# Performance work log

Hardware: AMD Instinct MI355X
Metric: run time of the kernel (lower is better)

Reference implementation:

```python
import jax, jax.numpy as jnp
from jax import lax
import numpy as np

B, T, NX, NXS, NY, NYS, H = 4096, 60, 4, 3, 4, 3, 128


def lstm(x, h0, c0, Wih, Whh, bih, bhh):
    """PyTorch-convention LSTM. x: [B,T,D] -> (hs [B,T,H], hT, cT). Gate order i,f,g,o."""
    xg = jnp.einsum('btd,gd->btg', x, Wih) + bih  # [B,T,4H] precomputed input gates

    def step(carry, xg_t):
        h, c = carry
        g = xg_t + h @ Whh.T + bhh
        i, f, gg, o = jnp.split(g, 4, axis=-1)
        c = jax.nn.sigmoid(f) * c + jax.nn.sigmoid(i) * jnp.tanh(gg)
        h = jax.nn.sigmoid(o) * jnp.tanh(c)
        return (h, c), h

    (hT, cT), hs = lax.scan(step, (h0, c0), jnp.swapaxes(xg, 0, 1))
    return jnp.swapaxes(hs, 0, 1), hT, cT


def setup_inputs() -> dict:
    key = jax.random.key(0)
    ks = jax.random.split(key, 24)
    s = 0.1  # weight init scale
    inp = {
        'inputs_main': jax.random.normal(ks[0], (B, T, NX), jnp.float32),
        'inputs_sfc': jax.random.normal(ks[1], (B, NXS), jnp.float32),
        'rnn1_mem': jax.random.normal(ks[2], (B, T, H), jnp.float32),
        'hx2': jax.random.normal(ks[3], (B, H), jnp.float32),
        'cx2': jax.random.normal(ks[4], (B, H), jnp.float32),
        # surface MLPs -> initial h/c of rnn1
        'W_sfc1': s * jax.random.normal(ks[5], (H, NXS), jnp.float32),
        'b_sfc1': s * jax.random.normal(ks[6], (H,), jnp.float32),
        'W_sfc2': s * jax.random.normal(ks[7], (H, NXS), jnp.float32),
        'b_sfc2': s * jax.random.normal(ks[8], (H,), jnp.float32),
        # rnn1: input dim nx + nh_mem = 4 + 128 = 132
        'Wih1': s * jax.random.normal(ks[9], (4 * H, NX + H), jnp.float32),
        'Whh1': s * jax.random.normal(ks[10], (4 * H, H), jnp.float32),
        'bih1': s * jax.random.normal(ks[11], (4 * H,), jnp.float32),
        'bhh1': s * jax.random.normal(ks[12], (4 * H,), jnp.float32),
        # rnn2: input dim H
        'Wih2': s * jax.random.normal(ks[13], (4 * H, H), jnp.float32),
        'Whh2': s * jax.random.normal(ks[14], (4 * H, H), jnp.float32),
        'bih2': s * jax.random.normal(ks[15], (4 * H,), jnp.float32),
        'bhh2': s * jax.random.normal(ks[16], (4 * H,), jnp.float32),
        # intermediate + output MLPs
        'W_lat': s * jax.random.normal(ks[17], (H, H), jnp.float32),
        'b_lat': s * jax.random.normal(ks[18], (H,), jnp.float32),
        'W_out': s * jax.random.normal(ks[19], (NY, H), jnp.float32),
        'b_out': s * jax.random.normal(ks[20], (NY,), jnp.float32),
        'W_so': s * jax.random.normal(ks[21], (NYS, H), jnp.float32),
        'b_so': s * jax.random.normal(ks[22], (NYS,), jnp.float32),
    }
    return inp


def reference(inputs_main, inputs_sfc, rnn1_mem, hx2, cx2,
              W_sfc1, b_sfc1, W_sfc2, b_sfc2,
              Wih1, Whh1, bih1, bhh1,
              Wih2, Whh2, bih2, bhh2,
              W_lat, b_lat, W_out, b_out, W_so, b_so):
    # initial states of rnn1 from surface features
    hx = jnp.tanh(inputs_sfc @ W_sfc1.T + b_sfc1)
    cx = jnp.tanh(inputs_sfc @ W_sfc2.T + b_sfc2)
    # flip vertical levels, concat memory feedback
    x = jnp.flip(inputs_main, axis=1)
    x = jnp.concatenate([x, rnn1_mem], axis=2)  # [B,T,NX+H]
    rnn1out, _, _ = lstm(x, hx, cx, Wih1, Whh1, bih1, bhh1)
    rnn1out = jnp.flip(rnn1out, axis=1)
    # second LSTM over the opposite direction, random initial state
    rnn2out, last_h, _ = lstm(rnn1out, hx2, cx2, Wih2, Whh2, bih2, bhh2)
    # intermediate mlp (also becomes next-step memory in the stateful module)
    lat = rnn2out @ W_lat.T + b_lat  # [B,T,H]
    out = lat @ W_out.T + b_out      # [B,T,NY]
    out_sfc = last_h @ W_so.T + b_so  # [B,NYS]
    return out, out_sfc
```

## Files before the change

kernel.cpp:

```cpp
#include <hip/hip_runtime.h>
#include <stdint.h>


typedef __bf16 bf16x8 __attribute__((ext_vector_type(8)));
typedef __bf16 bf16x4 __attribute__((ext_vector_type(4)));
typedef float  f32x4  __attribute__((ext_vector_type(4)));

#define HQ      4096u
#define H0_OFF  0u
#define XD_OFF  8192u
#define XA_OFF  16384u
#define HIST    24064u
#define LDS_SZ  163328
#define NWS     26

#define S1f (-1.4426950408889634f)
#define S2f (-2.8853900817779268f)

__device__ __forceinline__ bf16x8 ldw8s(const float* __restrict__ p, float s){
  float4 a = *(const float4*)p;
  float4 b = *(const float4*)(p+4);
  bf16x8 r;
  r[0]=(__bf16)(a.x*s); r[1]=(__bf16)(a.y*s); r[2]=(__bf16)(a.z*s); r[3]=(__bf16)(a.w*s);
  r[4]=(__bf16)(b.x*s); r[5]=(__bf16)(b.y*s); r[6]=(__bf16)(b.z*s); r[7]=(__bf16)(b.w*s);
  return r;
}
__device__ __forceinline__ void load_wgate(bf16x8 (&dst)[8], const float* pih, const float* phh, int gg, float s){
  #pragma unroll
  for (int kk=0;kk<4;++kk) dst[kk]   = ldw8s(pih + kk*32 + gg*8, s);
  #pragma unroll
  for (int kk=0;kk<4;++kk) dst[4+kk] = ldw8s(phh + kk*32 + gg*8, s);
}
__device__ __forceinline__ void step_barrier(){
  asm volatile("s_waitcnt lgkmcnt(0)\n\ts_barrier" ::: "memory");
}
__device__ __forceinline__ void lstm_pw(const f32x4& a0, const f32x4& a1,
                                        const f32x4& a2, const f32x4& a3,
                                        float (&c_)[4], float (&hn)[4]){
  #pragma unroll
  for (int i=0;i<4;++i){
    float ei = __builtin_amdgcn_exp2f(a0[i]);
    float ef = __builtin_amdgcn_exp2f(a1[i]);
    float eg = __builtin_amdgcn_exp2f(fminf(a2[i], 126.0f));
    float eo = __builtin_amdgcn_exp2f(a3[i]);
    float sf = __builtin_amdgcn_rcpf(1.0f + ef);
    float itg = (1.0f - eg) * __builtin_amdgcn_rcpf((1.0f + ei)*(1.0f + eg));
    float ci = sf*c_[i] + itg;
    float ec = __builtin_amdgcn_exp2f(S2f*__builtin_fabsf(ci));
    float th = (1.0f - ec) * __builtin_amdgcn_rcpf((1.0f + eo)*(1.0f + ec));
    c_[i] = ci;
    hn[i] = __builtin_copysignf(th, ci);
  }
}

__global__ void comb_kernel(const float* __restrict__ W_lat, const float* __restrict__ b_lat,
                            const float* __restrict__ W_out, const float* __restrict__ b_out,
                            float* __restrict__ wcomb){
  int tid = threadIdx.x;
  int m = tid >> 7, k = tid & 127;
  float s = 0.f;
  for (int a=0;a<128;++a) s += W_out[m*128+a]*W_lat[a*128+k];
  wcomb[tid] = s;
  if (tid < 4){
    float sb = b_out[tid];
    for (int a=0;a<128;++a) sb += W_out[tid*128+a]*b_lat[a];
    wcomb[512+tid] = sb;
  }
}

#define MFMA4(BASE, K0) \
  { _Pragma("unroll") \
    for (int kk=0;kk<4;++kk){ \
      uint4 q = *(const uint4*)(lds + (BASE) + ((abase + 64u*(uint32_t)kk) ^ amask)); \
      bf16x8 af = __builtin_bit_cast(bf16x8, q); \
      a0 = __builtin_amdgcn_mfma_f32_16x16x32_bf16(af, wB0[kk+(K0)], a0, 0,0,0); \
      a1 = __builtin_amdgcn_mfma_f32_16x16x32_bf16(af, wB1[kk+(K0)], a1, 0,0,0); \
      a2 = __builtin_amdgcn_mfma_f32_16x16x32_bf16(af, wB2[kk+(K0)], a2, 0,0,0); \
      a3 = __builtin_amdgcn_mfma_f32_16x16x32_bf16(af, wB3[kk+(K0)], a3, 0,0,0); \
    } }

__global__ __launch_bounds__(512, 2)
void lstm_fused(const float* __restrict__ xmain_g, const float* __restrict__ sfc,
                const float* __restrict__ mem_g, const float* __restrict__ hx2g,
                const float* __restrict__ cx2g,
                const float* __restrict__ Wsfc1, const float* __restrict__ bsfc1,
                const float* __restrict__ Wsfc2, const float* __restrict__ bsfc2,
                const float* __restrict__ Wih1, const float* __restrict__ Whh1,
                const float* __restrict__ bih1, const float* __restrict__ bhh1,
                const float* __restrict__ Wih2, const float* __restrict__ Whh2,
                const float* __restrict__ bih2, const float* __restrict__ bhh2,
                const float* __restrict__ Wso, const float* __restrict__ bso,
                const float* __restrict__ wcomb_ws,
                uint2* __restrict__ ws_u2, float* __restrict__ dout)
{
  __shared__ __align__(16) unsigned char lds[LDS_SZ];
  const int tid = threadIdx.x;
  const int w   = tid >> 6;
  const int l   = tid & 63;
  const int gg  = l >> 4;
  const int l16 = l & 15;
  const int blk = blockIdx.x;
  const int b0  = blk * 16;
  const int j   = (w<<4) + l16;
  const uint32_t amask = (uint32_t)((l16 & 7) << 4);
  const uint32_t abase = (uint32_t)(l16*256 + gg*16);
  const int srow = tid >> 5;
  const uint32_t stg_off = (uint32_t)(((srow*256) + (tid&31)*8) ^ ((srow&7)<<4));
  uint32_t hw_off[4];
  #pragma unroll
  for (int i=0;i<4;++i){
    int r = gg*4 + i;
    hw_off[i] = (uint32_t)((r*256 + j*2) ^ ((r&7)<<4));
  }
  const size_t ws_base = (size_t)blk * NWS * 512;

  #pragma unroll
  for (int e = tid; e < 960; e += 512){
    int t = e >> 4, row = e & 15;
    float4 xv = *(const float4*)(xmain_g + (size_t)(b0+row)*240 + t*4);
    bf16x4 b4; b4[0]=(__bf16)xv.x; b4[1]=(__bf16)xv.y; b4[2]=(__bf16)xv.z; b4[3]=(__bf16)xv.w;
    *(bf16x4*)(lds + XA_OFF + (uint32_t)e*8u) = b4;
  }
  const float* memrow = mem_g + (size_t)(b0 + srow)*7680 + (tid&31)*4;
  {
    float4 mv = *(const float4*)memrow;
    bf16x4 m4; m4[0]=(__bf16)mv.x; m4[1]=(__bf16)mv.y; m4[2]=(__bf16)mv.z; m4[3]=(__bf16)mv.w;
    *(bf16x4*)(lds + XD_OFF + stg_off) = m4;
  }
  {
    int c0 = (tid&31)*4;
    float4 wa = *(const float4*)(Wsfc1 + c0*3);
    float4 wb = *(const float4*)(Wsfc1 + c0*3 + 4);
    float4 wc = *(const float4*)(Wsfc1 + c0*3 + 8);
    const float* sp = sfc + (size_t)(b0+srow)*3;
    float s0 = sp[0], s1 = sp[1], s2 = sp[2];
    float4 bb = *(const float4*)(bsfc1 + c0);
    float v0 = tanhf(bb.x + s0*wa.x + s1*wa.y + s2*wa.z);
    float v1 = tanhf(bb.y + s0*wa.w + s1*wb.x + s2*wb.y);
    float v2 = tanhf(bb.z + s0*wb.z + s1*wb.w + s2*wc.x);
    float v3 = tanhf(bb.w + s0*wc.y + s1*wc.z + s2*wc.w);
    bf16x4 h4; h4[0]=(__bf16)v0; h4[1]=(__bf16)v1; h4[2]=(__bf16)v2; h4[3]=(__bf16)v3;
    *(bf16x4*)(lds + H0_OFF + stg_off) = h4;
  }
  float c_[4];
  {
    const float* wr = Wsfc2 + j*3;
    float w0_=wr[0], w1_=wr[1], w2_=wr[2];
    float bj = bsfc2[j];
    #pragma unroll
    for (int i=0;i<4;++i){
      const float* sp = sfc + (size_t)(b0 + gg*4 + i)*3;
      c_[i] = tanhf(bj + sp[0]*w0_ + sp[1]*w1_ + sp[2]*w2_);
    }
  }
  bf16x8 wB0[8], wB1[8], wB2[8], wB3[8];
  load_wgate(wB0, Wih1 + 4 + (size_t)(0*128+j)*132, Whh1 + (size_t)(0*128+j)*128, gg, S1f);
  load_wgate(wB1, Wih1 + 4 + (size_t)(1*128+j)*132, Whh1 + (size_t)(1*128+j)*128, gg, S1f);
  load_wgate(wB2, Wih1 + 4 + (size_t)(2*128+j)*132, Whh1 + (size_t)(2*128+j)*128, gg, S2f);
  load_wgate(wB3, Wih1 + 4 + (size_t)(3*128+j)*132, Whh1 + (size_t)(3*128+j)*128, gg, S1f);
  bf16x8 wxB0 = {}, wxB1 = {}, wxB2 = {}, wxB3 = {};
  if (gg == 0){
    float4 x0 = *(const float4*)(Wih1 + (size_t)(0*128+j)*132);
    float4 x1 = *(const float4*)(Wih1 + (size_t)(1*128+j)*132);
    float4 x2 = *(const float4*)(Wih1 + (size_t)(2*128+j)*132);
    float4 x3 = *(const float4*)(Wih1 + (size_t)(3*128+j)*132);
    wxB0[0]=(__bf16)(x0.x*S1f); wxB0[1]=(__bf16)(x0.y*S1f); wxB0[2]=(__bf16)(x0.z*S1f); wxB0[3]=(__bf16)(x0.w*S1f);
    wxB1[0]=(__bf16)(x1.x*S1f); wxB1[1]=(__bf16)(x1.y*S1f); wxB1[2]=(__bf16)(x1.z*S1f); wxB1[3]=(__bf16)(x1.w*S1f);
    wxB2[0]=(__bf16)(x2.x*S2f); wxB2[1]=(__bf16)(x2.y*S2f); wxB2[2]=(__bf16)(x2.z*S2f); wxB2[3]=(__bf16)(x2.w*S2f);
    wxB3[0]=(__bf16)(x3.x*S1f); wxB3[1]=(__bf16)(x3.y*S1f); wxB3[2]=(__bf16)(x3.z*S1f); wxB3[3]=(__bf16)(x3.w*S1f);
  }
  float bias0 = (bih1[0*128+j] + bhh1[0*128+j])*S1f;
  float bias1 = (bih1[1*128+j] + bhh1[1*128+j])*S1f;
  float bias2 = (bih1[2*128+j] + bhh1[2*128+j])*S2f;
  float bias3 = (bih1[3*128+j] + bhh1[3*128+j])*S1f;
  float4 P0 = *(const float4*)(memrow + 128);
  step_barrier();

  #pragma unroll 1
  for (int t=0; t<60; ++t){
    const uint32_t cur = (uint32_t)(t & 1), nxt = cur ^ 1u;
    const uint32_t Hc = H0_OFF + cur*HQ;
    const uint32_t xbase = (t >= NWS) ? (HIST + (uint32_t)(t-NWS)*HQ) : (XD_OFF + cur*HQ);
    float4 P1;
    if (t+2 < 60) P1 = *(const float4*)(memrow + (size_t)(t+2)*128);
    if (t > 0){
      uint2 hv = *(const uint2*)(lds + Hc + stg_off);
      if (t <= NWS) ws_u2[ws_base + (size_t)(t-1)*512 + tid] = hv;
      else *(uint2*)(lds + HIST + (uint32_t)(t-1-NWS)*HQ + stg_off) = hv;
    }
    const int tt = 59 - t;
    bf16x8 xa = {};
    if (gg == 0){
      bf16x4 x4 = *(const bf16x4*)(lds + XA_OFF + (uint32_t)((tt<<4) + l16)*8u);
      xa[0]=x4[0]; xa[1]=x4[1]; xa[2]=x4[2]; xa[3]=x4[3];
    }
    f32x4 a0 = {bias0,bias0,bias0,bias0};
    f32x4 a1 = {bias1,bias1,bias1,bias1};
    f32x4 a2 = {bias2,bias2,bias2,bias2};
    f32x4 a3 = {bias3,bias3,bias3,bias3};
    a0 = __builtin_amdgcn_mfma_f32_16x16x32_bf16(xa, wxB0, a0, 0,0,0);
    a1 = __builtin_amdgcn_mfma_f32_16x16x32_bf16(xa, wxB1, a1, 0,0,0);
    a2 = __builtin_amdgcn_mfma_f32_16x16x32_bf16(xa, wxB2, a2, 0,0,0);
    a3 = __builtin_amdgcn_mfma_f32_16x16x32_bf16(xa, wxB3, a3, 0,0,0);
    MFMA4(xbase, 0)
    MFMA4(Hc, 4)
    float hn[4];
    lstm_pw(a0, a1, a2, a3, c_, hn);
    if (t < 59){
      const uint32_t sdst = (t+1 >= NWS) ? (HIST + (uint32_t)(t+1-NWS)*HQ) : (XD_OFF + nxt*HQ);
      bf16x4 m4; m4[0]=(__bf16)P0.x; m4[1]=(__bf16)P0.y; m4[2]=(__bf16)P0.z; m4[3]=(__bf16)P0.w;
      *(bf16x4*)(lds + sdst + stg_off) = m4;
    }
    #pragma unroll
    for (int i=0;i<4;++i)
      *(__bf16*)(lds + H0_OFF + nxt*HQ + hw_off[i]) = (__bf16)hn[i];
    P0 = P1;
    step_barrier();
  }
  {
    uint2 hv = *(const uint2*)(lds + H0_OFF + stg_off);
    *(uint2*)(lds + HIST + 33u*HQ + stg_off) = hv;
    float4 h2v = *(const float4*)(hx2g + (size_t)(b0+srow)*128 + (tid&31)*4);
    bf16x4 h4; h4[0]=(__bf16)h2v.x; h4[1]=(__bf16)h2v.y; h4[2]=(__bf16)h2v.z; h4[3]=(__bf16)h2v.w;
    *(bf16x4*)(lds + H0_OFF + stg_off) = h4;
  }
  #pragma unroll
  for (int i=0;i<4;++i) c_[i] = cx2g[(size_t)(b0 + gg*4 + i)*128 + j];
  load_wgate(wB0, Wih2 + (size_t)(0*128+j)*128, Whh2 + (size_t)(0*128+j)*128, gg, S1f);
  load_wgate(wB1, Wih2 + (size_t)(1*128+j)*128, Whh2 + (size_t)(1*128+j)*128, gg, S1f);
  load_wgate(wB2, Wih2 + (size_t)(2*128+j)*128, Whh2 + (size_t)(2*128+j)*128, gg, S2f);
  load_wgate(wB3, Wih2 + (size_t)(3*128+j)*128, Whh2 + (size_t)(3*128+j)*128, gg, S1f);
  float nb0 = (bih2[0*128+j] + bhh2[0*128+j])*S1f;
  float nb1 = (bih2[1*128+j] + bhh2[1*128+j])*S1f;
  float nb2 = (bih2[2*128+j] + bhh2[2*128+j])*S2f;
  float nb3 = (bih2[3*128+j] + bhh2[3*128+j])*S1f;
  bias0=nb0; bias1=nb1; bias2=nb2; bias3=nb3;
  bf16x8 wcB[4] = {};
  if (w == 0){
    #pragma unroll
    for (int kk=0;kk<4;++kk){
      bf16x8 v = {};
      if (l16 < 4) v = ldw8s(wcomb_ws + l16*128 + kk*32 + gg*8, 1.0f);
      wcB[kk] = v;
    }
  }
  const float bc = (l16 < 4) ? wcomb_ws[512 + l16] : 0.f;
  asm volatile("s_waitcnt vmcnt(0) lgkmcnt(0)" ::: "memory");
  __builtin_amdgcn_s_barrier();

  uint2 P0u, P1u;
  #pragma unroll 1
  for (int t=0; t<60; ++t){
    const uint32_t cur = (uint32_t)(t & 1), nxt = cur ^ 1u;
    const uint32_t Hc = H0_OFF + cur*HQ;
    const int s = 59 - t;
    const uint32_t xbase = (s >= NWS) ? (HIST + (uint32_t)(s-NWS)*HQ) : (XD_OFF + cur*HQ);
    if (t >= 32 && t < 58) P1u = ws_u2[ws_base + (size_t)(57-t)*512 + tid];
    f32x4 a0 = {bias0,bias0,bias0,bias0};
    f32x4 a1 = {bias1,bias1,bias1,bias1};
    f32x4 a2 = {bias2,bias2,bias2,bias2};
    f32x4 a3 = {bias3,bias3,bias3,bias3};
    f32x4 ao = {0.f,0.f,0.f,0.f};
    MFMA4(xbase, 0)
    bf16x8 hf[4];
    #pragma unroll
    for (int kk=0;kk<4;++kk){
      uint4 q = *(const uint4*)(lds + Hc + ((abase + 64u*(uint32_t)kk) ^ amask));
      hf[kk] = __builtin_bit_cast(bf16x8, q);
    }
    #pragma unroll
    for (int kk=0;kk<4;++kk){
      a0 = __builtin_amdgcn_mfma_f32_16x16x32_bf16(hf[kk], wB0[kk+4], a0, 0,0,0);
      a1 = __builtin_amdgcn_mfma_f32_16x16x32_bf16(hf[kk], wB1[kk+4], a1, 0,0,0);
      a2 = __builtin_amdgcn_mfma_f32_16x16x32_bf16(hf[kk], wB2[kk+4], a2, 0,0,0);
      a3 = __builtin_amdgcn_mfma_f32_16x16x32_bf16(hf[kk], wB3[kk+4], a3, 0,0,0);
    }
    if (w == 0){
      #pragma unroll
      for (int kk=0;kk<4;++kk)
        ao = __builtin_amdgcn_mfma_f32_16x16x32_bf16(hf[kk], wcB[kk], ao, 0,0,0);
    }
    float hn[4];
    lstm_pw(a0, a1, a2, a3, c_, hn);
    if (t > 0 && w == 0 && l16 < 4){
      #pragma unroll
      for (int i=0;i<4;++i)
        dout[(size_t)(b0 + gg*4 + i)*240 + (size_t)(t-1)*4 + l16] = ao[i] + bc;
    }
    if (t >= 33 && t < 59)
      *(uint2*)(lds + XD_OFF + nxt*HQ + stg_off) = P0u;
    #pragma unroll
    for (int i=0;i<4;++i)
      *(__bf16*)(lds + H0_OFF + nxt*HQ + hw_off[i]) = (__bf16)hn[i];
    P0u = P1u;
    step_barrier();
  }

  if (w == 0){
    bf16x8 wsB[4];
    #pragma unroll
    for (int kk=0;kk<4;++kk){
      bf16x8 v = {};
      if (l16 < 3) v = ldw8s(Wso + l16*128 + kk*32 + gg*8, 1.0f);
      wsB[kk] = v;
    }
    f32x4 ao = {0.f,0.f,0.f,0.f};
    f32x4 as_ = {0.f,0.f,0.f,0.f};
    #pragma unroll
    for (int kk=0;kk<4;++kk){
      uint4 q = *(const uint4*)(lds + H0_OFF + ((abase + 64u*(uint32_t)kk) ^ amask));
      bf16x8 af = __builtin_bit_cast(bf16x8, q);
      ao  = __builtin_amdgcn_mfma_f32_16x16x32_bf16(af, wcB[kk], ao, 0,0,0);
      as_ = __builtin_amdgcn_mfma_f32_16x16x32_bf16(af, wsB[kk], as_, 0,0,0);
    }
    if (l16 < 4){
      #pragma unroll
      for (int i=0;i<4;++i)
        dout[(size_t)(b0 + gg*4 + i)*240 + 59*4 + l16] = ao[i] + bc;
    }
    if (l16 < 3){
      float bs = bso[l16];
      #pragma unroll
      for (int i=0;i<4;++i)
        dout[983040 + (size_t)(b0 + gg*4 + i)*3 + l16] = as_[i] + bs;
    }
  }
}

extern "C" void kernel_launch(void* const* d_in, const int* in_sizes, int n_in,
                              void* d_out, int out_size, void* d_ws, size_t ws_size,
                              hipStream_t stream){
  const float* inputs_main = (const float*)d_in[0];
  const float* inputs_sfc  = (const float*)d_in[1];
  const float* rnn1_mem    = (const float*)d_in[2];
  const float* hx2  = (const float*)d_in[3];
  const float* cx2  = (const float*)d_in[4];
  const float* W_sfc1 = (const float*)d_in[5];
  const float* b_sfc1 = (const float*)d_in[6];
  const float* W_sfc2 = (const float*)d_in[7];
  const float* b_sfc2 = (const float*)d_in[8];
  const float* Wih1 = (const float*)d_in[9];
  const float* Whh1 = (const float*)d_in[10];
  const float* bih1 = (const float*)d_in[11];
  const float* bhh1 = (const float*)d_in[12];
  const float* Wih2 = (const float*)d_in[13];
  const float* Whh2 = (const float*)d_in[14];
  const float* bih2 = (const float*)d_in[15];
  const float* bhh2 = (const float*)d_in[16];
  const float* W_lat = (const float*)d_in[17];
  const float* b_lat = (const float*)d_in[18];
  const float* W_out = (const float*)d_in[19];
  const float* b_out = (const float*)d_in[20];
  const float* W_so  = (const float*)d_in[21];
  const float* b_so  = (const float*)d_in[22];
  float* out = (float*)d_out;
  uint2* ws_u2 = (uint2*)d_ws;
  float* wcomb = (float*)((char*)d_ws + 62914560u);

  comb_kernel<<<dim3(1), dim3(512), 0, stream>>>(W_lat, b_lat, W_out, b_out, wcomb);
  lstm_fused<<<dim3(256), dim3(512), 0, stream>>>(inputs_main, inputs_sfc, rnn1_mem, hx2, cx2,
      W_sfc1, b_sfc1, W_sfc2, b_sfc2, Wih1, Whh1, bih1, bhh1, Wih2, Whh2, bih2, bhh2,
      W_so, b_so, wcomb, ws_u2, out);
}
```

Measured before the change: 194.2 us.

## Software-pipeline input-gate MFMAs one step ahead of the recurrent path

Restructures both LSTM time loops so the input-projection MFMAs for step t+1 are issued during step t, while the recurrent h@Whh MFMAs and the pointwise math for step t run. Accumulators are double-buffered in registers and the loop is unrolled by two. To make room, the x-staging ring grows from 2 to 4 slots, LDS offsets and the workspace split (NWS) shift, and memory prefetch moves two steps ahead. The aim is to take the input GEMM off the serial dependency chain, at the cost of more registers and more complex indexing, which could hurt occupancy.

```diff
diff --git a/kernel.cpp b/kernel.cpp
--- a/kernel.cpp
+++ b/kernel.cpp
@@ -9,10 +9,10 @@
 #define HQ      4096u
 #define H0_OFF  0u
 #define XD_OFF  8192u
-#define XA_OFF  16384u
-#define HIST    24064u
+#define XA_OFF  24576u
+#define HIST    32256u
 #define LDS_SZ  163328
-#define NWS     26
+#define NWS     28
 
 #define S1f (-1.4426950408889634f)
 #define S2f (-2.8853900817779268f)
@@ -68,16 +68,113 @@
   }
 }
 
-#define MFMA4(BASE, K0) \
-  { _Pragma("unroll") \
-    for (int kk=0;kk<4;++kk){ \
-      uint4 q = *(const uint4*)(lds + (BASE) + ((abase + 64u*(uint32_t)kk) ^ amask)); \
-      bf16x8 af = __builtin_bit_cast(bf16x8, q); \
-      a0 = __builtin_amdgcn_mfma_f32_16x16x32_bf16(af, wB0[kk+(K0)], a0, 0,0,0); \
-      a1 = __builtin_amdgcn_mfma_f32_16x16x32_bf16(af, wB1[kk+(K0)], a1, 0,0,0); \
-      a2 = __builtin_amdgcn_mfma_f32_16x16x32_bf16(af, wB2[kk+(K0)], a2, 0,0,0); \
-      a3 = __builtin_amdgcn_mfma_f32_16x16x32_bf16(af, wB3[kk+(K0)], a3, 0,0,0); \
-    } }
+#define MF(af_,wb_,ac_) ac_ = __builtin_amdgcn_mfma_f32_16x16x32_bf16(af_, wb_, ac_, 0,0,0)
+
+#define XPART1(A0_,A1_,A2_,A3_, XB_, TT_) do{ \
+    bf16x8 xa_ = {}; \
+    if (gg == 0){ bf16x4 x4_ = *(const bf16x4*)(lds + XA_OFF + (uint32_t)((((TT_))<<4)+l16)*8u); \
+      xa_[0]=x4_[0]; xa_[1]=x4_[1]; xa_[2]=x4_[2]; xa_[3]=x4_[3]; } \
+    A0_ = (f32x4){bias0,bias0,bias0,bias0}; \
+    A1_ = (f32x4){bias1,bias1,bias1,bias1}; \
+    A2_ = (f32x4){bias2,bias2,bias2,bias2}; \
+    A3_ = (f32x4){bias3,bias3,bias3,bias3}; \
+    MF(xa_,wxB0,A0_); MF(xa_,wxB1,A1_); MF(xa_,wxB2,A2_); MF(xa_,wxB3,A3_); \
+    _Pragma("unroll") \
+    for (int kk_=0;kk_<4;++kk_){ \
+      uint4 q_ = *(const uint4*)(lds + (XB_) + ((abase + 64u*(uint32_t)kk_) ^ amask)); \
+      bf16x8 af_ = __builtin_bit_cast(bf16x8, q_); \
+      MF(af_,wB0[kk_],A0_); MF(af_,wB1[kk_],A1_); MF(af_,wB2[kk_],A2_); MF(af_,wB3[kk_],A3_); } \
+  }while(0)
+
+#define XPART2(A0_,A1_,A2_,A3_, XB_) do{ \
+    A0_ = (f32x4){bias0,bias0,bias0,bias0}; \
+    A1_ = (f32x4){bias1,bias1,bias1,bias1}; \
+    A2_ = (f32x4){bias2,bias2,bias2,bias2}; \
+    A3_ = (f32x4){bias3,bias3,bias3,bias3}; \
+    _Pragma("unroll") \
+    for (int kk_=0;kk_<4;++kk_){ \
+      uint4 q_ = *(const uint4*)(lds + (XB_) + ((abase + 64u*(uint32_t)kk_) ^ amask)); \
+      bf16x8 af_ = __builtin_bit_cast(bf16x8, q_); \
+      MF(af_,wB0[kk_],A0_); MF(af_,wB1[kk_],A1_); MF(af_,wB2[kk_],A2_); MF(af_,wB3[kk_],A3_); } \
+  }while(0)
+
+#define BODY1(T_, CUR_, C0,C1,C2,C3, N0,N1,N2,N3) { \
+    const uint32_t Hc_ = H0_OFF + (uint32_t)(CUR_)*HQ; \
+    uint4 qh0_ = *(const uint4*)(lds + Hc_ + ((abase       ) ^ amask)); \
+    uint4 qh1_ = *(const uint4*)(lds + Hc_ + ((abase +  64u) ^ amask)); \
+    uint4 qh2_ = *(const uint4*)(lds + Hc_ + ((abase + 128u) ^ amask)); \
+    uint4 qh3_ = *(const uint4*)(lds + Hc_ + ((abase + 192u) ^ amask)); \
+    uint2 hv_ = *(const uint2*)(lds + Hc_ + stg_off); \
+    if ((T_) < 59){ \
+      const int s1_ = (T_) + 1; \
+      const uint32_t xb_ = (s1_ >= NWS) ? (HIST + (uint32_t)(s1_-NWS)*HQ) : (XD_OFF + (uint32_t)(s1_&3)*HQ); \
+      XPART1(N0,N1,N2,N3, xb_, 58-(T_)); \
+    } \
+    bf16x8 h0_ = __builtin_bit_cast(bf16x8, qh0_); \
+    bf16x8 h1_ = __builtin_bit_cast(bf16x8, qh1_); \
+    bf16x8 h2_ = __builtin_bit_cast(bf16x8, qh2_); \
+    bf16x8 h3_ = __builtin_bit_cast(bf16x8, qh3_); \
+    MF(h0_,wB0[4],C0); MF(h0_,wB1[4],C1); MF(h0_,wB2[4],C2); MF(h0_,wB3[4],C3); \
+    MF(h1_,wB0[5],C0); MF(h1_,wB1[5],C1); MF(h1_,wB2[5],C2); MF(h1_,wB3[5],C3); \
+    MF(h2_,wB0[6],C0); MF(h2_,wB1[6],C1); MF(h2_,wB2[6],C2); MF(h2_,wB3[6],C3); \
+    MF(h3_,wB0[7],C0); MF(h3_,wB1[7],C1); MF(h3_,wB2[7],C2); MF(h3_,wB3[7],C3); \
+    float hn_[4]; \
+    lstm_pw(C0,C1,C2,C3, c_, hn_); \
+    if ((T_) >= 1){ \
+      if ((T_) <= NWS) ws_u2[ws_base + (size_t)((T_)-1)*512 + tid] = hv_; \
+      else *(uint2*)(lds + HIST + (uint32_t)((T_)-1-NWS)*HQ + stg_off) = hv_; \
+    } \
+    if ((T_) + 2 <= 59){ \
+      const int s2_ = (T_) + 2; \
+      const uint32_t sd_ = (s2_ >= NWS) ? (HIST + (uint32_t)(s2_-NWS)*HQ) : (XD_OFF + (uint32_t)(s2_&3)*HQ); \
+      bf16x4 m4_; m4_[0]=(__bf16)P0.x; m4_[1]=(__bf16)P0.y; m4_[2]=(__bf16)P0.z; m4_[3]=(__bf16)P0.w; \
+      *(bf16x4*)(lds + sd_ + stg_off) = m4_; \
+    } \
+    _Pragma("unroll") \
+    for (int i_=0;i_<4;++i_) \
+      *(__bf16*)(lds + H0_OFF + (uint32_t)(1-(CUR_))*HQ + hw_off[i_]) = (__bf16)hn_[i_]; \
+    P0 = P1; \
+    if ((T_) + 4 <= 59) P1 = *(const float4*)(memrow + (size_t)((T_)+4)*128); \
+    step_barrier(); \
+  }
+
+#define BODY2(T_, CUR_, C0,C1,C2,C3, N0,N1,N2,N3) { \
+    const uint32_t Hc_ = H0_OFF + (uint32_t)(CUR_)*HQ; \
+    uint4 qh0_ = *(const uint4*)(lds + Hc_ + ((abase       ) ^ amask)); \
+    uint4 qh1_ = *(const uint4*)(lds + Hc_ + ((abase +  64u) ^ amask)); \
+    uint4 qh2_ = *(const uint4*)(lds + Hc_ + ((abase + 128u) ^ amask)); \
+    uint4 qh3_ = *(const uint4*)(lds + Hc_ + ((abase + 192u) ^ amask)); \
+    if ((T_) < 59){ \
+      const int s1_ = 58 - (T_); \
+      const uint32_t xb_ = (s1_ >= NWS) ? (HIST + (uint32_t)(s1_-NWS)*HQ) : (XD_OFF + (uint32_t)(s1_&3)*HQ); \
+      XPART2(N0,N1,N2,N3, xb_); \
+    } \
+    bf16x8 h0_ = __builtin_bit_cast(bf16x8, qh0_); \
+    bf16x8 h1_ = __builtin_bit_cast(bf16x8, qh1_); \
+    bf16x8 h2_ = __builtin_bit_cast(bf16x8, qh2_); \
+    bf16x8 h3_ = __builtin_bit_cast(bf16x8, qh3_); \
+    MF(h0_,wB0[4],C0); MF(h0_,wB1[4],C1); MF(h0_,wB2[4],C2); MF(h0_,wB3[4],C3); \
+    MF(h1_,wB0[5],C0); MF(h1_,wB1[5],C1); MF(h1_,wB2[5],C2); MF(h1_,wB3[5],C3); \
+    MF(h2_,wB0[6],C0); MF(h2_,wB1[6],C1); MF(h2_,wB2[6],C2); MF(h2_,wB3[6],C3); \
+    MF(h3_,wB0[7],C0); MF(h3_,wB1[7],C1); MF(h3_,wB2[7],C2); MF(h3_,wB3[7],C3); \
+    f32x4 ao_ = {0.f,0.f,0.f,0.f}; \
+    if (w == 0){ MF(h0_,wcB[0],ao_); MF(h1_,wcB[1],ao_); MF(h2_,wcB[2],ao_); MF(h3_,wcB[3],ao_); } \
+    float hn_[4]; \
+    lstm_pw(C0,C1,C2,C3, c_, hn_); \
+    if ((T_) > 0 && w == 0 && l16 < 4){ \
+      _Pragma("unroll") \
+      for (int i_=0;i_<4;++i_) \
+        dout[(size_t)(b0 + gg*4 + i_)*240 + (size_t)((T_)-1)*4 + l16] = ao_[i_] + bc; \
+    } \
+    if ((T_) >= 29 && (T_) <= 56) \
+      *(uint2*)(lds + XD_OFF + (uint32_t)((56-(T_))&3)*HQ + stg_off) = P0u; \
+    _Pragma("unroll") \
+    for (int i_=0;i_<4;++i_) \
+      *(__bf16*)(lds + H0_OFF + (uint32_t)(1-(CUR_))*HQ + hw_off[i_]) = (__bf16)hn_[i_]; \
+    P0u = P1u; \
+    if ((T_) >= 27 && (T_) <= 54) P1u = ws_u2[ws_base + (size_t)(54-(T_))*512 + tid]; \
+    step_barrier(); \
+  }
 
 __global__ __launch_bounds__(512, 2)
 void lstm_fused(const float* __restrict__ xmain_g, const float* __restrict__ sfc,
@@ -123,9 +220,12 @@
   }
   const float* memrow = mem_g + (size_t)(b0 + srow)*7680 + (tid&31)*4;
   {
-    float4 mv = *(const float4*)memrow;
-    bf16x4 m4; m4[0]=(__bf16)mv.x; m4[1]=(__bf16)mv.y; m4[2]=(__bf16)mv.z; m4[3]=(__bf16)mv.w;
-    *(bf16x4*)(lds + XD_OFF + stg_off) = m4;
+    float4 m0 = *(const float4*)memrow;
+    float4 m1 = *(const float4*)(memrow + 128);
+    bf16x4 a4; a4[0]=(__bf16)m0.x; a4[1]=(__bf16)m0.y; a4[2]=(__bf16)m0.z; a4[3]=(__bf16)m0.w;
+    bf16x4 b4; b4[0]=(__bf16)m1.x; b4[1]=(__bf16)m1.y; b4[2]=(__bf16)m1.z; b4[3]=(__bf16)m1.w;
+    *(bf16x4*)(lds + XD_OFF + stg_off) = a4;
+    *(bf16x4*)(lds + XD_OFF + HQ + stg_off) = b4;
   }
   {
     int c0 = (tid&31)*4;
@@ -173,53 +273,21 @@
   float bias1 = (bih1[1*128+j] + bhh1[1*128+j])*S1f;
   float bias2 = (bih1[2*128+j] + bhh1[2*128+j])*S2f;
   float bias3 = (bih1[3*128+j] + bhh1[3*128+j])*S1f;
-  float4 P0 = *(const float4*)(memrow + 128);
+  float4 P0 = *(const float4*)(memrow + 2*128);
+  float4 P1 = *(const float4*)(memrow + 3*128);
   step_barrier();
 
+  f32x4 A0, A1, A2, A3, B0, B1, B2, B3;
+  XPART1(A0,A1,A2,A3, XD_OFF, 59);
+
   #pragma unroll 1
-  for (int t=0; t<60; ++t){
-    const uint32_t cur = (uint32_t)(t & 1), nxt = cur ^ 1u;
-    const uint32_t Hc = H0_OFF + cur*HQ;
-    const uint32_t xbase = (t >= NWS) ? (HIST + (uint32_t)(t-NWS)*HQ) : (XD_OFF + cur*HQ);
-    float4 P1;
-    if (t+2 < 60) P1 = *(const float4*)(memrow + (size_t)(t+2)*128);
-    if (t > 0){
-      uint2 hv = *(const uint2*)(lds + Hc + stg_off);
-      if (t <= NWS) ws_u2[ws_base + (size_t)(t-1)*512 + tid] = hv;
-      else *(uint2*)(lds + HIST + (uint32_t)(t-1-NWS)*HQ + stg_off) = hv;
-    }
-    const int tt = 59 - t;
-    bf16x8 xa = {};
-    if (gg == 0){
-      bf16x4 x4 = *(const bf16x4*)(lds + XA_OFF + (uint32_t)((tt<<4) + l16)*8u);
-      xa[0]=x4[0]; xa[1]=x4[1]; xa[2]=x4[2]; xa[3]=x4[3];
-    }
-    f32x4 a0 = {bias0,bias0,bias0,bias0};
-    f32x4 a1 = {bias1,bias1,bias1,bias1};
-    f32x4 a2 = {bias2,bias2,bias2,bias2};
-    f32x4 a3 = {bias3,bias3,bias3,bias3};
-    a0 = __builtin_amdgcn_mfma_f32_16x16x32_bf16(xa, wxB0, a0, 0,0,0);
-    a1 = __builtin_amdgcn_mfma_f32_16x16x32_bf16(xa, wxB1, a1, 0,0,0);
-    a2 = __builtin_amdgcn_mfma_f32_16x16x32_bf16(xa, wxB2, a2, 0,0,0);
-    a3 = __builtin_amdgcn_mfma_f32_16x16x32_bf16(xa, wxB3, a3, 0,0,0);
-    MFMA4(xbase, 0)
-    MFMA4(Hc, 4)
-    float hn[4];
-    lstm_pw(a0, a1, a2, a3, c_, hn);
-    if (t < 59){
-      const uint32_t sdst = (t+1 >= NWS) ? (HIST + (uint32_t)(t+1-NWS)*HQ) : (XD_OFF + nxt*HQ);
-      bf16x4 m4; m4[0]=(__bf16)P0.x; m4[1]=(__bf16)P0.y; m4[2]=(__bf16)P0.z; m4[3]=(__bf16)P0.w;
-      *(bf16x4*)(lds + sdst + stg_off) = m4;
-    }
-    #pragma unroll
-    for (int i=0;i<4;++i)
-      *(__bf16*)(lds + H0_OFF + nxt*HQ + hw_off[i]) = (__bf16)hn[i];
-    P0 = P1;
-    step_barrier();
+  for (int tb = 0; tb < 60; tb += 2){
+    BODY1(tb,   0, A0,A1,A2,A3, B0,B1,B2,B3)
+    BODY1(tb+1, 1, B0,B1,B2,B3, A0,A1,A2,A3)
   }
   {
     uint2 hv = *(const uint2*)(lds + H0_OFF + stg_off);
-    *(uint2*)(lds + HIST + 33u*HQ + stg_off) = hv;
+    *(uint2*)(lds + HIST + 31u*HQ + stg_off) = hv;
     float4 h2v = *(const float4*)(hx2g + (size_t)(b0+srow)*128 + (tid&31)*4);
     bf16x4 h4; h4[0]=(__bf16)h2v.x; h4[1]=(__bf16)h2v.y; h4[2]=(__bf16)h2v.z; h4[3]=(__bf16)h2v.w;
     *(bf16x4*)(lds + H0_OFF + stg_off) = h4;
@@ -249,51 +317,12 @@
   __builtin_amdgcn_s_barrier();
 
   uint2 P0u, P1u;
+  XPART2(A0,A1,A2,A3, HIST + 31u*HQ);
+
   #pragma unroll 1
-  for (int t=0; t<60; ++t){
-    const uint32_t cur = (uint32_t)(t & 1), nxt = cur ^ 1u;
-    const uint32_t Hc = H0_OFF + cur*HQ;
-    const int s = 59 - t;
-    const uint32_t xbase = (s >= NWS) ? (HIST + (uint32_t)(s-NWS)*HQ) : (XD_OFF + cur*HQ);
-    if (t >= 32 && t < 58) P1u = ws_u2[ws_base + (size_t)(57-t)*512 + tid];
-    f32x4 a0 = {bias0,bias0,bias0,bias0};
-    f32x4 a1 = {bias1,bias1,bias1,bias1};
-    f32x4 a2 = {bias2,bias2,bias2,bias2};
-    f32x4 a3 = {bias3,bias3,bias3,bias3};
-    f32x4 ao = {0.f,0.f,0.f,0.f};
-    MFMA4(xbase, 0)
-    bf16x8 hf[4];
-    #pragma unroll
-    for (int kk=0;kk<4;++kk){
-      uint4 q = *(const uint4*)(lds + Hc + ((abase + 64u*(uint32_t)kk) ^ amask));
-      hf[kk] = __builtin_bit_cast(bf16x8, q);
-    }
-    #pragma unroll
-    for (int kk=0;kk<4;++kk){
-      a0 = __builtin_amdgcn_mfma_f32_16x16x32_bf16(hf[kk], wB0[kk+4], a0, 0,0,0);
-      a1 = __builtin_amdgcn_mfma_f32_16x16x32_bf16(hf[kk], wB1[kk+4], a1, 0,0,0);
-      a2 = __builtin_amdgcn_mfma_f32_16x16x32_bf16(hf[kk], wB2[kk+4], a2, 0,0,0);
-      a3 = __builtin_amdgcn_mfma_f32_16x16x32_bf16(hf[kk], wB3[kk+4], a3, 0,0,0);
-    }
-    if (w == 0){
-      #pragma unroll
-      for (int kk=0;kk<4;++kk)
-        ao = __builtin_amdgcn_mfma_f32_16x16x32_bf16(hf[kk], wcB[kk], ao, 0,0,0);
-    }
-    float hn[4];
-    lstm_pw(a0, a1, a2, a3, c_, hn);
-    if (t > 0 && w == 0 && l16 < 4){
-      #pragma unroll
-      for (int i=0;i<4;++i)
-        dout[(size_t)(b0 + gg*4 + i)*240 + (size_t)(t-1)*4 + l16] = ao[i] + bc;
-    }
-    if (t >= 33 && t < 59)
-      *(uint2*)(lds + XD_OFF + nxt*HQ + stg_off) = P0u;
-    #pragma unroll
-    for (int i=0;i<4;++i)
-      *(__bf16*)(lds + H0_OFF + nxt*HQ + hw_off[i]) = (__bf16)hn[i];
-    P0u = P1u;
-    step_barrier();
+  for (int tb = 0; tb < 60; tb += 2){
+    BODY2(tb,   0, A0,A1,A2,A3, B0,B1,B2,B3)
+    BODY2(tb+1, 1, B0,B1,B2,B3, A0,A1,A2,A3)
   }
 
   if (w == 0){
```

New measurement: 198.5 us. 1.02x slower.
